# Optimization experiments

Measured on AMD Instinct MI355X. Metric: run time of the kernel, lower is better.

Reference implementation:

```python
import jax, jax.numpy as jnp
import numpy as np
import math

B, S, D, H = 1, 2048, 2048, 16
HD = D // H  # head_dim = 128


def _rotate_half(x):
    h = x.shape[-1] // 2
    return jnp.concatenate([-x[..., h:], x[..., :h]], axis=-1)


def setup_inputs() -> dict:
    key = jax.random.key(0)
    ks = jax.random.split(key, 8)
    hidden_states = jax.random.normal(ks[0], (B, S, D), dtype=jnp.float32)
    # additive causal mask: 0 on/below diagonal, large negative above
    causal = jnp.tril(jnp.ones((S, S), dtype=bool))
    attention_mask = jnp.where(causal, 0.0, -1e9).astype(jnp.float32)[None, None]
    # LLaMA rotary tables for head_dim
    inv_freq = 1.0 / (10000.0 ** (jnp.arange(0, HD, 2, dtype=jnp.float32) / HD))
    t = jnp.arange(S, dtype=jnp.float32)
    freqs = jnp.einsum('s,d->sd', t, inv_freq)          # [S, HD/2]
    emb = jnp.concatenate([freqs, freqs], axis=-1)       # [S, HD]
    cos = jnp.cos(emb)[None, None]                       # [1,1,S,HD]
    sin = jnp.sin(emb)[None, None]
    scale = 1.0 / math.sqrt(D)
    Wq = jax.random.normal(ks[1], (D, D), dtype=jnp.float32) * scale
    Wk = jax.random.normal(ks[2], (D, D), dtype=jnp.float32) * scale
    Wv = jax.random.normal(ks[3], (D, D), dtype=jnp.float32) * scale
    Wo = jax.random.normal(ks[4], (D, D), dtype=jnp.float32) * scale
    # IA3 scales initialized to ones (as in module), perturbed slightly to be non-trivial
    l_k = jnp.ones((1, H, 1, HD), dtype=jnp.float32) + 0.01 * jax.random.normal(ks[5], (1, H, 1, HD), dtype=jnp.float32)
    l_v = jnp.ones((1, H, 1, HD), dtype=jnp.float32) + 0.01 * jax.random.normal(ks[6], (1, H, 1, HD), dtype=jnp.float32)
    return {
        'hidden_states': hidden_states, 'attention_mask': attention_mask,
        'cos': cos, 'sin': sin,
        'Wq': Wq, 'Wk': Wk, 'Wv': Wv, 'Wo': Wo, 'l_k': l_k, 'l_v': l_v,
    }


def reference(hidden_states, attention_mask, cos, sin, Wq, Wk, Wv, Wo, l_k, l_v):
    b, s, d = hidden_states.shape
    h, hd = H, HD
    # projections (nn.Linear: x @ W.T), split heads -> [b, h, s, hd]
    def split_heads(x):
        return x.reshape(b, s, h, hd).transpose(0, 2, 1, 3)
    q = split_heads(hidden_states @ Wq.T)
    k = split_heads(hidden_states @ Wk.T)
    v = split_heads(hidden_states @ Wv.T)
    # RoPE on q and k
    q = q * cos + _rotate_half(q) * sin
    k = k * cos + _rotate_half(k) * sin
    # IA3: note the module scales QUERY by peft_l_k and VALUE by peft_l_v
    q = q * l_k
    v = v * l_v
    # manual attention
    scores = jnp.einsum('bhqd,bhkd->bhqk', q, k) / math.sqrt(hd)
    scores = scores + attention_mask
    attn = jax.nn.softmax(scores.astype(jnp.float32), axis=-1).astype(scores.dtype)
    out = jnp.einsum('bhqk,bhkd->bhqd', attn, v)
    out = out.transpose(0, 2, 1, 3).reshape(b, s, d)
    return out @ Wo.T
```

## Files before the change

### kernel.cpp

```cpp
#include <hip/hip_runtime.h>

typedef __attribute__((ext_vector_type(8))) short short8;
typedef __attribute__((ext_vector_type(4))) float f32x4;
typedef unsigned short ushort;

#define S_LEN 2048
#define D_MODEL 2048
#define NH 16
#define HD 128

__device__ __forceinline__ float b2f(ushort u) {
  union { unsigned int i; float f; } v; v.i = ((unsigned int)u) << 16; return v.f;
}
__device__ __forceinline__ ushort f2b(float f) {
  union { float f; unsigned int i; } v; v.f = f;
  unsigned int r = v.i + 0x7FFFu + ((v.i >> 16) & 1u);
  return (ushort)(r >> 16);
}

__device__ __forceinline__ void gload_lds16(const void* g, void* l) {
  __builtin_amdgcn_global_load_lds(
      (const __attribute__((address_space(1))) void*)g,
      (__attribute__((address_space(3))) void*)l, 16, 0, 0);
}

template<bool C32>
__device__ __forceinline__ void gemm_bf16_body(const ushort* __restrict__ A,
                                               const ushort* __restrict__ B,
                                               void* __restrict__ Cp, int ldc)
{
  __shared__ ushort lA[128 * 64];
  __shared__ ushort lB[128 * 64];
  const int tid  = threadIdx.x;
  const int lane = tid & 63;
  const int wave = tid >> 6;
  const int quad = lane >> 4;
  const int l15  = lane & 15;
  const int wm   = wave >> 1;
  const int wn   = wave & 1;
  const int m0   = blockIdx.y * 128;
  const int n0   = blockIdx.x * 128;

  f32x4 acc[4][4];
#pragma unroll
  for (int i = 0; i < 4; ++i)
#pragma unroll
    for (int j = 0; j < 4; ++j)
      acc[i][j] = (f32x4){0.f, 0.f, 0.f, 0.f};

  const int srow0 = wave * 8 + (lane >> 3);
  const int cph   = lane & 7;

  for (int kt = 0; kt < 32; ++kt) {
    __syncthreads();
#pragma unroll
    for (int j = 0; j < 4; ++j) {
      const int row = j * 32 + srow0;
      const int gc  = cph ^ (row & 7);
      gload_lds16(A + (size_t)(m0 + row) * 2048 + kt * 64 + gc * 8,
                  &lA[row * 64 + cph * 8]);
      gload_lds16(B + (size_t)(n0 + row) * 2048 + kt * 64 + gc * 8,
                  &lB[row * 64 + cph * 8]);
    }
    __syncthreads();
#pragma unroll
    for (int kk = 0; kk < 2; ++kk) {
      short8 af[4], bfr[4];
#pragma unroll
      for (int i = 0; i < 4; ++i) {
        const int r = wm * 64 + i * 16 + l15;
        af[i] = *(const short8*)&lA[r * 64 + (((kk * 4 + quad) ^ (l15 & 7)) * 8)];
      }
#pragma unroll
      for (int j = 0; j < 4; ++j) {
        const int r = wn * 64 + j * 16 + l15;
        bfr[j] = *(const short8*)&lB[r * 64 + (((kk * 4 + quad) ^ (l15 & 7)) * 8)];
      }
#pragma unroll
      for (int i = 0; i < 4; ++i)
#pragma unroll
        for (int j = 0; j < 4; ++j)
          acc[i][j] = __builtin_amdgcn_mfma_f32_16x16x32_bf16(af[i], bfr[j], acc[i][j], 0, 0, 0);
    }
  }

#pragma unroll
  for (int i = 0; i < 4; ++i)
#pragma unroll
    for (int j = 0; j < 4; ++j)
#pragma unroll
      for (int r = 0; r < 4; ++r) {
        const int row = m0 + wm * 64 + i * 16 + quad * 4 + r;
        const int col = n0 + wn * 64 + j * 16 + l15;
        if (C32) ((float*)Cp)[(size_t)row * ldc + col] = acc[i][j][r];
        else     ((ushort*)Cp)[(size_t)row * ldc + col] = f2b(acc[i][j][r]);
      }
}

__global__ __launch_bounds__(256)
void gemm_bf16_b(const ushort* __restrict__ A, const ushort* __restrict__ B,
                 ushort* __restrict__ C, int ldc)
{ gemm_bf16_body<false>(A, B, C, ldc); }

__global__ __launch_bounds__(256)
void gemm_bf16_f(const ushort* __restrict__ A, const ushort* __restrict__ B,
                 float* __restrict__ C, int ldc)
{ gemm_bf16_body<true>(A, B, C, ldc); }

__global__ __launch_bounds__(256)
void cvt_to_bf16(const float* __restrict__ hs, const float* __restrict__ Wq,
                 const float* __restrict__ Wk, const float* __restrict__ Wv,
                 const float* __restrict__ Wo, ushort* __restrict__ dst)
{
  const size_t base = ((size_t)blockIdx.x * 256 + threadIdx.x) * 8;
  const int row = (int)(base >> 11);
  const int col = (int)(base & 2047);
  const float* src;
  if      (row < 2048) src = Wq + (size_t)row * 2048;
  else if (row < 4096) src = Wk + (size_t)(row - 2048) * 2048;
  else if (row < 6144) src = Wv + (size_t)(row - 4096) * 2048;
  else if (row < 8192) src = Wo + (size_t)(row - 6144) * 2048;
  else                 src = hs + (size_t)(row - 8192) * 2048;
  float4 a = *(const float4*)(src + col);
  float4 b = *(const float4*)(src + col + 4);
  short8 s;
  s[0] = (short)f2b(a.x); s[1] = (short)f2b(a.y);
  s[2] = (short)f2b(a.z); s[3] = (short)f2b(a.w);
  s[4] = (short)f2b(b.x); s[5] = (short)f2b(b.y);
  s[6] = (short)f2b(b.z); s[7] = (short)f2b(b.w);
  *(short8*)(dst + base) = s;
}

template<bool A32, bool B32, bool C32>
__device__ __forceinline__ void gemm_body(const void* __restrict__ Ap,
                                          const void* __restrict__ Bp,
                                          void* __restrict__ Cp)
{
  __shared__ ushort lA[128 * 72];
  __shared__ ushort lB[128 * 72];
  const int tid  = threadIdx.x;
  const int lane = tid & 63;
  const int wave = tid >> 6;
  const int quad = lane >> 4;
  const int l15  = lane & 15;
  const int wm   = wave >> 1;
  const int wn   = wave & 1;
  const int m0   = blockIdx.y * 128;
  const int n0   = blockIdx.x * 128;

  f32x4 acc[4][4];
#pragma unroll
  for (int i = 0; i < 4; ++i)
#pragma unroll
    for (int j = 0; j < 4; ++j)
      acc[i][j] = (f32x4){0.f, 0.f, 0.f, 0.f};

  const int srow = tid >> 1;
  const int scol = (tid & 1) * 32;
  ushort* aL = &lA[srow * 72 + scol];
  ushort* bL = &lB[srow * 72 + scol];

  for (int kt = 0; kt < 32; ++kt) {
    __syncthreads();
    if (A32) {
      const float* g = (const float*)Ap + (size_t)(m0 + srow) * 2048 + kt * 64 + scol;
#pragma unroll
      for (int j = 0; j < 4; ++j) {
        float4 f0 = *(const float4*)(g + 8 * j);
        float4 f1 = *(const float4*)(g + 8 * j + 4);
        short8 sv;
        sv[0] = (short)f2b(f0.x); sv[1] = (short)f2b(f0.y);
        sv[2] = (short)f2b(f0.z); sv[3] = (short)f2b(f0.w);
        sv[4] = (short)f2b(f1.x); sv[5] = (short)f2b(f1.y);
        sv[6] = (short)f2b(f1.z); sv[7] = (short)f2b(f1.w);
        *(short8*)(aL + 8 * j) = sv;
      }
    } else {
      const ushort* g = (const ushort*)Ap + (size_t)(m0 + srow) * 2048 + kt * 64 + scol;
#pragma unroll
      for (int j = 0; j < 4; ++j)
        *(short8*)(aL + 8 * j) = *(const short8*)(g + 8 * j);
    }
    if (B32) {
      const float* g = (const float*)Bp + (size_t)(n0 + srow) * 2048 + kt * 64 + scol;
#pragma unroll
      for (int j = 0; j < 4; ++j) {
        float4 f0 = *(const float4*)(g + 8 * j);
        float4 f1 = *(const float4*)(g + 8 * j + 4);
        short8 sv;
        sv[0] = (short)f2b(f0.x); sv[1] = (short)f2b(f0.y);
        sv[2] = (short)f2b(f0.z); sv[3] = (short)f2b(f0.w);
        sv[4] = (short)f2b(f1.x); sv[5] = (short)f2b(f1.y);
        sv[6] = (short)f2b(f1.z); sv[7] = (short)f2b(f1.w);
        *(short8*)(bL + 8 * j) = sv;
      }
    } else {
      const ushort* g = (const ushort*)Bp + (size_t)(n0 + srow) * 2048 + kt * 64 + scol;
#pragma unroll
      for (int j = 0; j < 4; ++j)
        *(short8*)(bL + 8 * j) = *(const short8*)(g + 8 * j);
    }
    __syncthreads();
#pragma unroll
    for (int kk = 0; kk < 2; ++kk) {
      short8 af[4], bfr[4];
#pragma unroll
      for (int i = 0; i < 4; ++i)
        af[i] = *(const short8*)&lA[(wm * 64 + i * 16 + l15) * 72 + kk * 32 + quad * 8];
#pragma unroll
      for (int j = 0; j < 4; ++j)
        bfr[j] = *(const short8*)&lB[(wn * 64 + j * 16 + l15) * 72 + kk * 32 + quad * 8];
#pragma unroll
      for (int i = 0; i < 4; ++i)
#pragma unroll
        for (int j = 0; j < 4; ++j)
          acc[i][j] = __builtin_amdgcn_mfma_f32_16x16x32_bf16(af[i], bfr[j], acc[i][j], 0, 0, 0);
    }
  }

#pragma unroll
  for (int i = 0; i < 4; ++i)
#pragma unroll
    for (int j = 0; j < 4; ++j)
#pragma unroll
      for (int r = 0; r < 4; ++r) {
        const int row = m0 + wm * 64 + i * 16 + quad * 4 + r;
        const int col = n0 + wn * 64 + j * 16 + l15;
        if (C32) ((float*)Cp)[(size_t)row * 2048 + col] = acc[i][j][r];
        else     ((ushort*)Cp)[(size_t)row * 2048 + col] = f2b(acc[i][j][r]);
      }
}

__global__ __launch_bounds__(256)
void gemm_qkv_f32(const float* __restrict__ A, const float* __restrict__ Bq,
                  const float* __restrict__ Bk, const float* __restrict__ Bv,
                  ushort* __restrict__ Cq, ushort* __restrict__ Ck, ushort* __restrict__ Cv)
{
  const float* B = (blockIdx.z == 0) ? Bq : (blockIdx.z == 1 ? Bk : Bv);
  ushort* C      = (blockIdx.z == 0) ? Cq : (blockIdx.z == 1 ? Ck : Cv);
  gemm_body<true, true, false>(A, B, C);
}

__global__ __launch_bounds__(256)
void gemm_wo_f32(const ushort* __restrict__ A, const float* __restrict__ B,
                 float* __restrict__ C)
{ gemm_body<false, true, true>(A, B, C); }

__global__ __launch_bounds__(256)
void rope_ia3(ushort* __restrict__ base, int stride, int koff, int voff,
              const float* __restrict__ cosb, const float* __restrict__ sinb,
              const float* __restrict__ lk, const float* __restrict__ lv)
{
  const int s = blockIdx.x;
  const float qscale = 0.08838834764831845f * 1.4426950408889634f;
#pragma unroll
  for (int i = 0; i < 4; ++i) {
    const int p = threadIdx.x + 256 * i;
    const int h = p >> 6;
    const int d = p & 63;

    const size_t lo = (size_t)s * stride + h * HD + d;
    const size_t hi = lo + 64;
    const float c_lo = cosb[s * HD + d];
    const float c_hi = cosb[s * HD + d + 64];
    const float s_lo = sinb[s * HD + d];
    const float s_hi = sinb[s * HD + d + 64];

    ushort* Q = base;
    ushort* K = base + koff;
    ushort* V = base + voff;

    const float qlo = b2f(Q[lo]), qhi = b2f(Q[hi]);
    const float klo = b2f(K[lo]), khi = b2f(K[hi]);
    const float vlo = b2f(V[lo]), vhi = b2f(V[hi]);

    const float rq_lo = qlo * c_lo - qhi * s_lo;
    const float rq_hi = qhi * c_hi + qlo * s_hi;
    const float rk_lo = klo * c_lo - khi * s_lo;
    const float rk_hi = khi * c_hi + klo * s_hi;

    Q[lo] = f2b(rq_lo * lk[h * HD + d]      * qscale);
    Q[hi] = f2b(rq_hi * lk[h * HD + d + 64] * qscale);
    K[lo] = f2b(rk_lo);
    K[hi] = f2b(rk_hi);
    V[lo] = f2b(vlo * lv[h * HD + d]);
    V[hi] = f2b(vhi * lv[h * HD + d + 64]);
  }
}

__global__ __launch_bounds__(256)
void flash_attn(const ushort* __restrict__ QKV, int stride, int koff, int voff,
                ushort* __restrict__ Ob, int ostride)
{
  __shared__ ushort Kl[64 * 128];
  __shared__ ushort Vt[128 * 64];
  __shared__ ushort Pl[4][16 * 72];

  const int tid  = threadIdx.x;
  const int lane = tid & 63;
  const int w    = tid >> 6;
  const int quad = lane >> 4;
  const int l15  = lane & 15;
  const int qt   = (int)gridDim.x - 1 - (int)blockIdx.x;
  const int h    = blockIdx.y;

  const ushort* Q = QKV;
  const ushort* K = QKV + koff;
  const ushort* V = QKV + voff;

  const int qrow = qt * 64 + w * 16 + l15;
  short8 qa[4];
#pragma unroll
  for (int kk = 0; kk < 4; ++kk)
    qa[kk] = *(const short8*)(Q + (size_t)qrow * stride + h * HD + kk * 32 + quad * 8);

  float m_[4], l_[4];
  f32x4 o[8];
#pragma unroll
  for (int r = 0; r < 4; ++r) { m_[r] = -1e30f; l_[r] = 0.f; }
#pragma unroll
  for (int nf = 0; nf < 8; ++nf) o[nf] = (f32x4){0.f, 0.f, 0.f, 0.f};

  const int ksrow0 = w * 4 + (lane >> 4);
  const int kch    = lane & 15;
  const int vkp    = tid & 15;
  const int vd8    = tid >> 4;

  for (int kt = 0; kt <= qt; ++kt) {
    __syncthreads();

#pragma unroll
    for (int j = 0; j < 4; ++j) {
      const int row = j * 16 + ksrow0;
      const int gc  = kch ^ (row & 15);
      gload_lds16(K + (size_t)(kt * 64 + row) * stride + h * HD + gc * 8,
                  &Kl[row * 128 + kch * 8]);
    }

    {
      const ushort* vb = V + (size_t)(kt * 64) * stride + h * HD + vd8 * 8;
      short8 v0 = *(const short8*)(vb + (size_t)(2 * vkp)      * stride);
      short8 v1 = *(const short8*)(vb + (size_t)(2 * vkp + 1)  * stride);
      short8 v2 = *(const short8*)(vb + (size_t)(2 * vkp + 32) * stride);
      short8 v3 = *(const short8*)(vb + (size_t)(2 * vkp + 33) * stride);
      const int wlo = vkp >> 2, woff = 2 * (vkp & 3);
#pragma unroll
      for (int c = 0; c < 8; ++c) {
        const int d = vd8 * 8 + c;
        unsigned int p01 = (ushort)v0[c] | ((unsigned int)(ushort)v1[c] << 16);
        unsigned int p23 = (ushort)v2[c] | ((unsigned int)(ushort)v3[c] << 16);
        *(unsigned int*)&Vt[d * 64 + ((wlo       ^ c) * 8) + woff] = p01;
        *(unsigned int*)&Vt[d * 64 + (((wlo + 4) ^ c) * 8) + woff] = p23;
      }
    }
    __syncthreads();

    f32x4 sf[4];
#pragma unroll
    for (int n = 0; n < 4; ++n) sf[n] = (f32x4){0.f, 0.f, 0.f, 0.f};
#pragma unroll
    for (int kk = 0; kk < 4; ++kk)
#pragma unroll
      for (int n = 0; n < 4; ++n) {
        const int key = n * 16 + l15;
        short8 b = *(const short8*)&Kl[key * 128 + (((kk * 4 + quad) ^ l15) * 8)];
        sf[n] = __builtin_amdgcn_mfma_f32_16x16x32_bf16(qa[kk], b, sf[n], 0, 0, 0);
      }

    if (kt == qt) {
#pragma unroll
      for (int n = 0; n < 4; ++n)
#pragma unroll
        for (int r = 0; r < 4; ++r)
          if (n * 16 + l15 > w * 16 + quad * 4 + r) sf[n][r] = -1e30f;
    }

    float pm[4];
#pragma unroll
    for (int r = 0; r < 4; ++r)
      pm[r] = fmaxf(fmaxf(sf[0][r], sf[1][r]), fmaxf(sf[2][r], sf[3][r]));
#pragma unroll
    for (int off = 1; off < 16; off <<= 1)
#pragma unroll
      for (int r = 0; r < 4; ++r)
        pm[r] = fmaxf(pm[r], __shfl_xor(pm[r], off));

    float al[4], ps[4], p[4][4];
#pragma unroll
    for (int r = 0; r < 4; ++r) {
      const float mn = fmaxf(m_[r], pm[r]);
      al[r] = exp2f(m_[r] - mn);
      m_[r] = mn;
      ps[r] = 0.f;
    }
#pragma unroll
    for (int n = 0; n < 4; ++n)
#pragma unroll
      for (int r = 0; r < 4; ++r) {
        p[n][r] = exp2f(sf[n][r] - m_[r]);
        ps[r] += p[n][r];
      }
#pragma unroll
    for (int off = 1; off < 16; off <<= 1)
#pragma unroll
      for (int r = 0; r < 4; ++r)
        ps[r] += __shfl_xor(ps[r], off);
#pragma unroll
    for (int r = 0; r < 4; ++r) l_[r] = al[r] * l_[r] + ps[r];
#pragma unroll
    for (int nf = 0; nf < 8; ++nf)
#pragma unroll
      for (int r = 0; r < 4; ++r) o[nf][r] *= al[r];

#pragma unroll
    for (int n = 0; n < 4; ++n)
#pragma unroll
      for (int r = 0; r < 4; ++r)
        Pl[w][(quad * 4 + r) * 72 + n * 16 + l15] = f2b(p[n][r]);

#pragma unroll
    for (int kk = 0; kk < 2; ++kk) {
      short8 pa = *(const short8*)&Pl[w][l15 * 72 + kk * 32 + quad * 8];
#pragma unroll
      for (int nf = 0; nf < 8; ++nf) {
        const int d = nf * 16 + l15;
        short8 b = *(const short8*)&Vt[d * 64 + (((kk * 4 + quad) ^ (l15 & 7)) * 8)];
        o[nf] = __builtin_amdgcn_mfma_f32_16x16x32_bf16(pa, b, o[nf], 0, 0, 0);
      }
    }
  }

  float inv[4];
#pragma unroll
  for (int r = 0; r < 4; ++r) inv[r] = 1.0f / l_[r];
#pragma unroll
  for (int nf = 0; nf < 8; ++nf)
#pragma unroll
    for (int r = 0; r < 4; ++r) {
      const int row = qt * 64 + w * 16 + quad * 4 + r;
      const int col = h * HD + nf * 16 + l15;
      Ob[(size_t)row * ostride + col] = f2b(o[nf][r] * inv[r]);
    }
}

extern "C" void kernel_launch(void* const* d_in, const int* in_sizes, int n_in,
                              void* d_out, int out_size, void* d_ws, size_t ws_size,
                              hipStream_t stream)
{
  const float* hs   = (const float*)d_in[0];
  const float* cosb = (const float*)d_in[2];
  const float* sinb = (const float*)d_in[3];
  const float* Wq   = (const float*)d_in[4];
  const float* Wk   = (const float*)d_in[5];
  const float* Wv   = (const float*)d_in[6];
  const float* Wo   = (const float*)d_in[7];
  const float* lk   = (const float*)d_in[8];
  const float* lv   = (const float*)d_in[9];
  float* out = (float*)d_out;

  char* ws = (char*)d_ws;
  const bool fast = ws_size >= (size_t)64 * 1024 * 1024;

  if (fast) {
    ushort* WB  = (ushort*)ws;
    ushort* hsB = WB + (size_t)8192 * 2048;
    ushort* QKV = (ushort*)(ws + (size_t)40 * 1024 * 1024);
    ushort* Ab  = hsB;

    cvt_to_bf16<<<dim3(10240), 256, 0, stream>>>(hs, Wq, Wk, Wv, Wo, WB);
    gemm_bf16_b<<<dim3(48, 16), 256, 0, stream>>>(hsB, WB, QKV, 6144);
    rope_ia3<<<dim3(S_LEN), 256, 0, stream>>>(QKV, 6144, 2048, 4096, cosb, sinb, lk, lv);
    flash_attn<<<dim3(S_LEN / 64, NH), 256, 0, stream>>>(QKV, 6144, 2048, 4096, Ab, 2048);
    gemm_bf16_f<<<dim3(16, 16), 256, 0, stream>>>(Ab, WB + (size_t)6144 * 2048, out, 2048);
  } else {
    const size_t SZ = (size_t)S_LEN * D_MODEL;
    ushort* Qb = (ushort*)ws;
    ushort* Kb = Qb + SZ;
    ushort* Vb = Qb + 2 * SZ;
    ushort* Ab = Qb;

    gemm_qkv_f32<<<dim3(16, 16, 3), 256, 0, stream>>>(hs, Wq, Wk, Wv, Qb, Kb, Vb);
    rope_ia3<<<dim3(S_LEN), 256, 0, stream>>>(Qb, 2048, (int)SZ, (int)(2 * SZ), cosb, sinb, lk, lv);
    flash_attn<<<dim3(S_LEN / 64, NH), 256, 0, stream>>>(Qb, 2048, (int)SZ, (int)(2 * SZ), Ab, 2048);
    gemm_wo_f32<<<dim3(16, 16), 256, 0, stream>>>(Ab, Wo, out);
  }
}
```

Before: 352.6 us.

## Split long causal attention tiles across two blocks and pre-transpose V in QKV GEMM

The QKV GEMM epilogue now applies the IA3 value scale and writes V transposed (head-dim major) into the arena, so the attention kernel can load V^T tiles straight into LDS with async global-to-LDS loads instead of transposing them through registers. The flash attention grid is rebalanced: the 16 longest query tiles are split into two key-range chunks, each writing unnormalised partial outputs plus per-row max and sum, and a new combine kernel merges them. This evens out causal per-block work to cut tail latency, at the cost of an extra launch, partial-result traffic and bf16 rounding of the partials. RoPE no longer touches V.

```diff
diff --git a/kernel.cpp b/kernel.cpp
--- a/kernel.cpp
+++ b/kernel.cpp
@@ -1,6 +1,7 @@
 #include <hip/hip_runtime.h>
 
 typedef __attribute__((ext_vector_type(8))) short short8;
+typedef __attribute__((ext_vector_type(4))) short s16x4;
 typedef __attribute__((ext_vector_type(4))) float f32x4;
 typedef unsigned short ushort;
 
@@ -24,10 +25,11 @@
       (__attribute__((address_space(3))) void*)l, 16, 0, 0);
 }
 
-template<bool C32>
+template<bool C32, bool QKV>
 __device__ __forceinline__ void gemm_bf16_body(const ushort* __restrict__ A,
                                                const ushort* __restrict__ B,
-                                               void* __restrict__ Cp, int ldc)
+                                               void* __restrict__ Cp, int ldc,
+                                               const float* __restrict__ lv)
 {
   __shared__ ushort lA[128 * 64];
   __shared__ ushort lB[128 * 64];
@@ -84,6 +86,23 @@
     }
   }
 
+  if (QKV && n0 >= 4096) {
+    ushort* C = (ushort*)Cp;
+#pragma unroll
+    for (int j = 0; j < 4; ++j)
+#pragma unroll
+      for (int i = 0; i < 4; ++i) {
+        const int vcol = n0 - 4096 + wn * 64 + j * 16 + l15;
+        const float sc = lv[vcol];
+        const int sb   = m0 + wm * 64 + i * 16 + quad * 4;
+        s16x4 pk;
+#pragma unroll
+        for (int r = 0; r < 4; ++r) pk[r] = (short)f2b(acc[i][j][r] * sc);
+        *(s16x4*)&C[(size_t)vcol * 6144 + 4096 + sb] = pk;
+      }
+    return;
+  }
+
 #pragma unroll
   for (int i = 0; i < 4; ++i)
 #pragma unroll
@@ -98,14 +117,14 @@
 }
 
 __global__ __launch_bounds__(256)
-void gemm_bf16_b(const ushort* __restrict__ A, const ushort* __restrict__ B,
-                 ushort* __restrict__ C, int ldc)
-{ gemm_bf16_body<false>(A, B, C, ldc); }
+void gemm_qkv_b(const ushort* __restrict__ A, const ushort* __restrict__ B,
+                ushort* __restrict__ C, const float* __restrict__ lv)
+{ gemm_bf16_body<false, true>(A, B, C, 6144, lv); }
 
 __global__ __launch_bounds__(256)
 void gemm_bf16_f(const ushort* __restrict__ A, const ushort* __restrict__ B,
                  float* __restrict__ C, int ldc)
-{ gemm_bf16_body<true>(A, B, C, ldc); }
+{ gemm_bf16_body<true, false>(A, B, C, ldc, nullptr); }
 
 __global__ __launch_bounds__(256)
 void cvt_to_bf16(const float* __restrict__ hs, const float* __restrict__ Wq,
@@ -131,6 +150,245 @@
   *(short8*)(dst + base) = s;
 }
 
+__global__ __launch_bounds__(256)
+void rope_qk(ushort* __restrict__ arena,
+             const float* __restrict__ cosb, const float* __restrict__ sinb,
+             const float* __restrict__ lk)
+{
+  const int s = blockIdx.x;
+  const float qscale = 0.08838834764831845f * 1.4426950408889634f;
+#pragma unroll
+  for (int i = 0; i < 4; ++i) {
+    const int p = threadIdx.x + 256 * i;
+    const int h = p >> 6;
+    const int d = p & 63;
+
+    const size_t qlo_i = (size_t)s * 6144 + h * HD + d;
+    const size_t klo_i = qlo_i + 2048;
+    const float c_lo = cosb[s * HD + d];
+    const float c_hi = cosb[s * HD + d + 64];
+    const float s_lo = sinb[s * HD + d];
+    const float s_hi = sinb[s * HD + d + 64];
+
+    const float qlo = b2f(arena[qlo_i]), qhi = b2f(arena[qlo_i + 64]);
+    const float klo = b2f(arena[klo_i]), khi = b2f(arena[klo_i + 64]);
+
+    const float rq_lo = qlo * c_lo - qhi * s_lo;
+    const float rq_hi = qhi * c_hi + qlo * s_hi;
+    const float rk_lo = klo * c_lo - khi * s_lo;
+    const float rk_hi = khi * c_hi + klo * s_hi;
+
+    arena[qlo_i]      = f2b(rq_lo * lk[h * HD + d]      * qscale);
+    arena[qlo_i + 64] = f2b(rq_hi * lk[h * HD + d + 64] * qscale);
+    arena[klo_i]      = f2b(rk_lo);
+    arena[klo_i + 64] = f2b(rk_hi);
+  }
+}
+
+__global__ __launch_bounds__(256)
+void flash_attn_sk(const ushort* __restrict__ arena,
+                   ushort* __restrict__ Ab,
+                   ushort* __restrict__ Op,
+                   float* __restrict__ Ml)
+{
+  __shared__ ushort Kl[64 * 128];
+  __shared__ ushort Vt[128 * 64];
+  __shared__ ushort Pl[4][16 * 72];
+
+  const int tid  = threadIdx.x;
+  const int lane = tid & 63;
+  const int w    = tid >> 6;
+  const int quad = lane >> 4;
+  const int l15  = lane & 15;
+  const int h    = blockIdx.y;
+
+  const int idx = blockIdx.x;
+  int qt, ck; bool chunked;
+  if (idx < 32) { qt = 31 - (idx >> 1); ck = idx & 1; chunked = true; }
+  else          { qt = 47 - idx;        ck = 0;       chunked = false; }
+  const int ktBeg = chunked ? ck * 16 : 0;
+  const int ktEnd = (chunked && ck == 0) ? 16 : (qt + 1);
+
+  const int qrow = qt * 64 + w * 16 + l15;
+  short8 qa[4];
+#pragma unroll
+  for (int kk = 0; kk < 4; ++kk)
+    qa[kk] = *(const short8*)(arena + (size_t)qrow * 6144 + h * HD + kk * 32 + quad * 8);
+
+  float m_[4], l_[4];
+  f32x4 o[8];
+#pragma unroll
+  for (int r = 0; r < 4; ++r) { m_[r] = -1e30f; l_[r] = 0.f; }
+#pragma unroll
+  for (int nf = 0; nf < 8; ++nf) o[nf] = (f32x4){0.f, 0.f, 0.f, 0.f};
+
+  const int ksrow0 = w * 4 + (lane >> 4);
+  const int kch    = lane & 15;
+  const int vrow0  = w * 8 + (lane >> 3);
+  const int vch    = lane & 7;
+
+  for (int kt = ktBeg; kt < ktEnd; ++kt) {
+    __syncthreads();
+
+#pragma unroll
+    for (int j = 0; j < 4; ++j) {
+      const int row = j * 16 + ksrow0;
+      const int gc  = kch ^ (row & 15);
+      gload_lds16(arena + (size_t)(kt * 64 + row) * 6144 + 2048 + h * HD + gc * 8,
+                  &Kl[row * 128 + kch * 8]);
+    }
+#pragma unroll
+    for (int j = 0; j < 4; ++j) {
+      const int d  = j * 32 + vrow0;
+      const int gc = vch ^ (d & 7);
+      gload_lds16(arena + (size_t)(h * HD + d) * 6144 + 4096 + kt * 64 + gc * 8,
+                  &Vt[d * 64 + vch * 8]);
+    }
+    __syncthreads();
+
+    f32x4 sf[4];
+#pragma unroll
+    for (int n = 0; n < 4; ++n) sf[n] = (f32x4){0.f, 0.f, 0.f, 0.f};
+#pragma unroll
+    for (int kk = 0; kk < 4; ++kk)
+#pragma unroll
+      for (int n = 0; n < 4; ++n) {
+        const int key = n * 16 + l15;
+        short8 b = *(const short8*)&Kl[key * 128 + (((kk * 4 + quad) ^ l15) * 8)];
+        sf[n] = __builtin_amdgcn_mfma_f32_16x16x32_bf16(qa[kk], b, sf[n], 0, 0, 0);
+      }
+
+    if (kt == qt) {
+#pragma unroll
+      for (int n = 0; n < 4; ++n)
+#pragma unroll
+        for (int r = 0; r < 4; ++r)
+          if (n * 16 + l15 > w * 16 + quad * 4 + r) sf[n][r] = -1e30f;
+    }
+
+    float pm[4];
+#pragma unroll
+    for (int r = 0; r < 4; ++r)
+      pm[r] = fmaxf(fmaxf(sf[0][r], sf[1][r]), fmaxf(sf[2][r], sf[3][r]));
+#pragma unroll
+    for (int off = 1; off < 16; off <<= 1)
+#pragma unroll
+      for (int r = 0; r < 4; ++r)
+        pm[r] = fmaxf(pm[r], __shfl_xor(pm[r], off));
+
+    float al[4], ps[4], p[4][4];
+#pragma unroll
+    for (int r = 0; r < 4; ++r) {
+      const float mn = fmaxf(m_[r], pm[r]);
+      al[r] = exp2f(m_[r] - mn);
+      m_[r] = mn;
+      ps[r] = 0.f;
+    }
+#pragma unroll
+    for (int n = 0; n < 4; ++n)
+#pragma unroll
+      for (int r = 0; r < 4; ++r) {
+        p[n][r] = exp2f(sf[n][r] - m_[r]);
+        ps[r] += p[n][r];
+      }
+#pragma unroll
+    for (int off = 1; off < 16; off <<= 1)
+#pragma unroll
+      for (int r = 0; r < 4; ++r)
+        ps[r] += __shfl_xor(ps[r], off);
+#pragma unroll
+    for (int r = 0; r < 4; ++r) l_[r] = al[r] * l_[r] + ps[r];
+#pragma unroll
+    for (int nf = 0; nf < 8; ++nf)
+#pragma unroll
+      for (int r = 0; r < 4; ++r) o[nf][r] *= al[r];
+
+#pragma unroll
+    for (int n = 0; n < 4; ++n)
+#pragma unroll
+      for (int r = 0; r < 4; ++r)
+        Pl[w][(quad * 4 + r) * 72 + n * 16 + l15] = f2b(p[n][r]);
+
+#pragma unroll
+    for (int kk = 0; kk < 2; ++kk) {
+      short8 pa = *(const short8*)&Pl[w][l15 * 72 + kk * 32 + quad * 8];
+#pragma unroll
+      for (int nf = 0; nf < 8; ++nf) {
+        const int d = nf * 16 + l15;
+        short8 b = *(const short8*)&Vt[d * 64 + (((kk * 4 + quad) ^ (l15 & 7)) * 8)];
+        o[nf] = __builtin_amdgcn_mfma_f32_16x16x32_bf16(pa, b, o[nf], 0, 0, 0);
+      }
+    }
+  }
+
+  if (!chunked) {
+    float inv[4];
+#pragma unroll
+    for (int r = 0; r < 4; ++r) inv[r] = 1.0f / l_[r];
+#pragma unroll
+    for (int nf = 0; nf < 8; ++nf)
+#pragma unroll
+      for (int r = 0; r < 4; ++r) {
+        const int row = qt * 64 + w * 16 + quad * 4 + r;
+        const int col = h * HD + nf * 16 + l15;
+        Ab[(size_t)row * 2048 + col] = f2b(o[nf][r] * inv[r]);
+      }
+  } else {
+    const int pid = (qt - 16) * 2 + ck;
+    ushort* dst = Op + (size_t)(h * 32 + pid) * 64 * 128;
+#pragma unroll
+    for (int nf = 0; nf < 8; ++nf)
+#pragma unroll
+      for (int r = 0; r < 4; ++r) {
+        const int row = w * 16 + quad * 4 + r;
+        const int col = nf * 16 + l15;
+        dst[row * 128 + col] = f2b(o[nf][r]);
+      }
+    if (l15 == 0) {
+      float* mp = Ml + ((size_t)(h * 32 + pid) * 2 + 0) * 64;
+      float* lp = Ml + ((size_t)(h * 32 + pid) * 2 + 1) * 64;
+#pragma unroll
+      for (int r = 0; r < 4; ++r) {
+        mp[w * 16 + quad * 4 + r] = m_[r];
+        lp[w * 16 + quad * 4 + r] = l_[r];
+      }
+    }
+  }
+}
+
+__global__ __launch_bounds__(256)
+void fa_combine(const ushort* __restrict__ Op, const float* __restrict__ Ml,
+                ushort* __restrict__ Ab)
+{
+  const int qt = 16 + blockIdx.x;
+  const int h  = blockIdx.y;
+  const int r  = threadIdx.x >> 2;
+  const int c0 = (threadIdx.x & 3) * 32;
+  const int p0 = h * 32 + (qt - 16) * 2;
+  const int p1 = p0 + 1;
+  const float m0 = Ml[((size_t)p0 * 2 + 0) * 64 + r];
+  const float l0 = Ml[((size_t)p0 * 2 + 1) * 64 + r];
+  const float m1 = Ml[((size_t)p1 * 2 + 0) * 64 + r];
+  const float l1 = Ml[((size_t)p1 * 2 + 1) * 64 + r];
+  const float M  = fmaxf(m0, m1);
+  const float w0 = exp2f(m0 - M), w1 = exp2f(m1 - M);
+  const float inv = 1.0f / (w0 * l0 + w1 * l1);
+  const float a0 = w0 * inv, a1 = w1 * inv;
+  const ushort* s0 = Op + ((size_t)p0 * 64 + r) * 128 + c0;
+  const ushort* s1 = Op + ((size_t)p1 * 64 + r) * 128 + c0;
+  ushort* d = Ab + (size_t)(qt * 64 + r) * 2048 + h * 128 + c0;
+#pragma unroll
+  for (int j = 0; j < 4; ++j) {
+    short8 x0 = *(const short8*)(s0 + j * 8);
+    short8 x1 = *(const short8*)(s1 + j * 8);
+    short8 y;
+#pragma unroll
+    for (int e = 0; e < 8; ++e)
+      y[e] = (short)f2b(a0 * b2f((ushort)x0[e]) + a1 * b2f((ushort)x1[e]));
+    *(short8*)(d + j * 8) = y;
+  }
+}
+
 template<bool A32, bool B32, bool C32>
 __device__ __forceinline__ void gemm_body(const void* __restrict__ Ap,
                                           const void* __restrict__ Bp,
@@ -247,9 +505,9 @@
 { gemm_body<false, true, true>(A, B, C); }
 
 __global__ __launch_bounds__(256)
-void rope_ia3(ushort* __restrict__ base, int stride, int koff, int voff,
-              const float* __restrict__ cosb, const float* __restrict__ sinb,
-              const float* __restrict__ lk, const float* __restrict__ lv)
+void rope_ia3_old(ushort* __restrict__ base, int stride, int koff, int voff,
+                  const float* __restrict__ cosb, const float* __restrict__ sinb,
+                  const float* __restrict__ lk, const float* __restrict__ lv)
 {
   const int s = blockIdx.x;
   const float qscale = 0.08838834764831845f * 1.4426950408889634f;
@@ -258,27 +516,22 @@
     const int p = threadIdx.x + 256 * i;
     const int h = p >> 6;
     const int d = p & 63;
-
     const size_t lo = (size_t)s * stride + h * HD + d;
     const size_t hi = lo + 64;
     const float c_lo = cosb[s * HD + d];
     const float c_hi = cosb[s * HD + d + 64];
     const float s_lo = sinb[s * HD + d];
     const float s_hi = sinb[s * HD + d + 64];
-
     ushort* Q = base;
     ushort* K = base + koff;
     ushort* V = base + voff;
-
     const float qlo = b2f(Q[lo]), qhi = b2f(Q[hi]);
     const float klo = b2f(K[lo]), khi = b2f(K[hi]);
     const float vlo = b2f(V[lo]), vhi = b2f(V[hi]);
-
     const float rq_lo = qlo * c_lo - qhi * s_lo;
     const float rq_hi = qhi * c_hi + qlo * s_hi;
     const float rk_lo = klo * c_lo - khi * s_lo;
     const float rk_hi = khi * c_hi + klo * s_hi;
-
     Q[lo] = f2b(rq_lo * lk[h * HD + d]      * qscale);
     Q[hi] = f2b(rq_hi * lk[h * HD + d + 64] * qscale);
     K[lo] = f2b(rk_lo);
@@ -289,8 +542,8 @@
 }
 
 __global__ __launch_bounds__(256)
-void flash_attn(const ushort* __restrict__ QKV, int stride, int koff, int voff,
-                ushort* __restrict__ Ob, int ostride)
+void flash_attn_old(const ushort* __restrict__ QKV, int stride, int koff, int voff,
+                    ushort* __restrict__ Ob, int ostride)
 {
   __shared__ ushort Kl[64 * 128];
   __shared__ ushort Vt[128 * 64];
@@ -328,7 +581,6 @@
 
   for (int kt = 0; kt <= qt; ++kt) {
     __syncthreads();
-
 #pragma unroll
     for (int j = 0; j < 4; ++j) {
       const int row = j * 16 + ksrow0;
@@ -336,7 +588,6 @@
       gload_lds16(K + (size_t)(kt * 64 + row) * stride + h * HD + gc * 8,
                   &Kl[row * 128 + kch * 8]);
     }
-
     {
       const ushort* vb = V + (size_t)(kt * 64) * stride + h * HD + vd8 * 8;
       short8 v0 = *(const short8*)(vb + (size_t)(2 * vkp)      * stride);
@@ -466,11 +717,14 @@
     ushort* hsB = WB + (size_t)8192 * 2048;
     ushort* QKV = (ushort*)(ws + (size_t)40 * 1024 * 1024);
     ushort* Ab  = hsB;
+    ushort* Op  = WB;
+    float*  Ml  = (float*)(ws + (size_t)8 * 1024 * 1024);
 
     cvt_to_bf16<<<dim3(10240), 256, 0, stream>>>(hs, Wq, Wk, Wv, Wo, WB);
-    gemm_bf16_b<<<dim3(48, 16), 256, 0, stream>>>(hsB, WB, QKV, 6144);
-    rope_ia3<<<dim3(S_LEN), 256, 0, stream>>>(QKV, 6144, 2048, 4096, cosb, sinb, lk, lv);
-    flash_attn<<<dim3(S_LEN / 64, NH), 256, 0, stream>>>(QKV, 6144, 2048, 4096, Ab, 2048);
+    gemm_qkv_b<<<dim3(48, 16), 256, 0, stream>>>(hsB, WB, QKV, lv);
+    rope_qk<<<dim3(S_LEN), 256, 0, stream>>>(QKV, cosb, sinb, lk);
+    flash_attn_sk<<<dim3(48, NH), 256, 0, stream>>>(QKV, Ab, Op, Ml);
+    fa_combine<<<dim3(16, NH), 256, 0, stream>>>(Op, Ml, Ab);
     gemm_bf16_f<<<dim3(16, 16), 256, 0, stream>>>(Ab, WB + (size_t)6144 * 2048, out, 2048);
   } else {
     const size_t SZ = (size_t)S_LEN * D_MODEL;
@@ -480,8 +734,8 @@
     ushort* Ab = Qb;
 
     gemm_qkv_f32<<<dim3(16, 16, 3), 256, 0, stream>>>(hs, Wq, Wk, Wv, Qb, Kb, Vb);
-    rope_ia3<<<dim3(S_LEN), 256, 0, stream>>>(Qb, 2048, (int)SZ, (int)(2 * SZ), cosb, sinb, lk, lv);
-    flash_attn<<<dim3(S_LEN / 64, NH), 256, 0, stream>>>(Qb, 2048, (int)SZ, (int)(2 * SZ), Ab, 2048);
+    rope_ia3_old<<<dim3(S_LEN), 256, 0, stream>>>(Qb, 2048, (int)SZ, (int)(2 * SZ), cosb, sinb, lk, lv);
+    flash_attn_old<<<dim3(S_LEN / 64, NH), 256, 0, stream>>>(Qb, 2048, (int)SZ, (int)(2 * SZ), Ab, 2048);
     gemm_wo_f32<<<dim3(16, 16), 256, 0, stream>>>(Ab, Wo, out);
   }
 }
```

Result: no change. 348.9 us (-1.0%).
